# Kernel tuning notes

Measured on AMD Instinct MI355X. Metric: run time of the kernel, lower is better.

The kernel has to match this reference:

```python
import jax, jax.numpy as jnp
import numpy as np

B, S, D = 4, 4096, 512
H = 8
DH = D // H


def setup_inputs() -> dict:
    key = jax.random.key(0)
    k = jax.random.split(key, 5)
    x = jax.random.normal(k[0], (B, S, D), dtype=jnp.float32)
    # in_proj: Linear(D, 3D) with bias; out_proj: Linear(D, D) with bias
    std = 1.0 / np.sqrt(D)
    w_in = jax.random.uniform(k[1], (3 * D, D), minval=-std, maxval=std, dtype=jnp.float32)
    b_in = jax.random.uniform(k[2], (3 * D,), minval=-std, maxval=std, dtype=jnp.float32)
    w_out = jax.random.uniform(k[3], (D, D), minval=-std, maxval=std, dtype=jnp.float32)
    b_out = jax.random.uniform(k[4], (D,), minval=-std, maxval=std, dtype=jnp.float32)
    return {"x": x, "w_in": w_in, "b_in": b_in, "w_out": w_out, "b_out": b_out}


def reference(x, w_in, b_in, w_out, b_out):
    batch, seq_len, d_embed = x.shape
    scale = DH ** 0.5
    qkv = jnp.einsum('bsd,ed->bse', x, w_in) + b_in  # (B, S, 3D)
    q, k, v = jnp.split(qkv, 3, axis=-1)
    # (B, H, S, DH)
    q = q.reshape(batch, seq_len, H, DH).transpose(0, 2, 1, 3)
    k = k.reshape(batch, seq_len, H, DH).transpose(0, 2, 1, 3)
    v = v.reshape(batch, seq_len, H, DH).transpose(0, 2, 1, 3)
    scores = jnp.einsum('bhqd,bhkd->bhqk', q, k) / scale  # full N x N scores
    weights = jax.nn.softmax(scores, axis=-1)
    out = jnp.einsum('bhqk,bhkd->bhqd', weights, v)
    out = out.transpose(0, 2, 1, 3).reshape(batch, seq_len, d_embed)
    out = jnp.einsum('bsd,ed->bse', out, w_out) + b_out
    return out
```

## Files before the change

### kernel.cpp

```cpp
#include <hip/hip_runtime.h>
#include <hip/hip_bf16.h>

typedef short short8 __attribute__((ext_vector_type(8)));
typedef unsigned short ushort8v __attribute__((ext_vector_type(8)));
typedef unsigned short ushort4v __attribute__((ext_vector_type(4)));
typedef float f32x4 __attribute__((ext_vector_type(4)));
typedef unsigned int uint32;

#define USH unsigned short

__device__ __forceinline__ USH f2bf(float f) {
  unsigned int u = __builtin_bit_cast(unsigned int, f);
  u = (u + 0x7FFFu + ((u >> 16) & 1u)) >> 16;
  return (USH)u;
}

__device__ __forceinline__ uint32 pkbf2(float lo, float hi) {
  __hip_bfloat162 h2 = __float22bfloat162_rn(float2{lo, hi});
  uint32 r;
  __builtin_memcpy(&r, &h2, 4);
  return r;
}

__device__ __forceinline__ f32x4 mfma16(short8 a, short8 b, f32x4 c) {
  return __builtin_amdgcn_mfma_f32_16x16x32_bf16(a, b, c, 0, 0, 0);
}

__device__ __forceinline__ void gload16(const USH* g, USH* l) {
  __builtin_amdgcn_global_load_lds(
      (const __attribute__((address_space(1))) unsigned int*)g,
      (__attribute__((address_space(3))) unsigned int*)l, 16, 0, 0);
}

template <int CTRL>
__device__ __forceinline__ float dppmaxstep(float x) {
  int xi = __builtin_bit_cast(int, x);
  int yi = __builtin_amdgcn_update_dpp(xi, xi, CTRL, 0xF, 0xF, true);
  return fmaxf(x, __builtin_bit_cast(float, yi));
}
__device__ __forceinline__ float rowmax16(float x) {
  x = dppmaxstep<0xB1>(x);
  x = dppmaxstep<0x4E>(x);
  x = dppmaxstep<0x141>(x);
  x = dppmaxstep<0x140>(x);
  return x;
}

__device__ __forceinline__ f32x4 vmax4(f32x4 a, f32x4 b) {
  f32x4 r;
  r[0] = fmaxf(a[0], b[0]);
  r[1] = fmaxf(a[1], b[1]);
  r[2] = fmaxf(a[2], b[2]);
  r[3] = fmaxf(a[3], b[3]);
  return r;
}

__global__ __launch_bounds__(256) void cvt_bf16(const float* __restrict__ in,
                                                USH* __restrict__ out, int n4) {
  int i = blockIdx.x * 256 + threadIdx.x;
  if (i >= n4) return;
  f32x4 v = *(const f32x4*)(in + (size_t)i * 4);
  ushort4v o;
#pragma unroll
  for (int k = 0; k < 4; k++) o[k] = f2bf(v[k]);
  *(ushort4v*)(out + (size_t)i * 4) = o;
}

template <bool OUT_F32>
__global__ __launch_bounds__(256) void gemm_bt(const USH* __restrict__ A,
                                               const USH* __restrict__ B,
                                               const float* __restrict__ bias,
                                               void* __restrict__ Cout,
                                               int M, int N, int K) {
  __shared__ __align__(16) USH As[128 * 64];
  __shared__ __align__(16) USH Bs[128 * 64];
  const int tid = threadIdx.x;
  const int row0 = blockIdx.x * 128;
  const int col0 = blockIdx.y * 128;
  const int wid = tid >> 6, lane = tid & 63;
  const int wr = (wid >> 1) * 64, wc = (wid & 1) * 64;
  const int lmod = lane & 15, ldiv = lane >> 4;
  const int asw = lmod & 7;
  const int srow = lane >> 3;
  const int scol = ((lane & 7) ^ srow) * 8;

  f32x4 acc[4][4];
#pragma unroll
  for (int i = 0; i < 4; i++)
#pragma unroll
    for (int j = 0; j < 4; j++) acc[i][j] = (f32x4){0.f, 0.f, 0.f, 0.f};

  const USH* Ab = A + (size_t)row0 * K;
  const USH* Bb = B + (size_t)col0 * K;

  for (int k0 = 0; k0 < K; k0 += 64) {
    __syncthreads();
#pragma unroll
    for (int i = 0; i < 4; i++) {
      int r0 = wid * 32 + i * 8;
      int r = r0 + srow;
      gload16(&Ab[(size_t)r * K + k0 + scol], &As[r0 * 64]);
      gload16(&Bb[(size_t)r * K + k0 + scol], &Bs[r0 * 64]);
    }
    __syncthreads();
#pragma unroll
    for (int kk = 0; kk < 64; kk += 32) {
      short8 a[4], b[4];
#pragma unroll
      for (int i = 0; i < 4; i++)
        a[i] = *(const short8*)&As[(wr + i * 16 + lmod) * 64 +
                                   ((((kk >> 3) + ldiv) ^ asw) << 3)];
#pragma unroll
      for (int i = 0; i < 4; i++)
        b[i] = *(const short8*)&Bs[(wc + i * 16 + lmod) * 64 +
                                   ((((kk >> 3) + ldiv) ^ asw) << 3)];
#pragma unroll
      for (int i = 0; i < 4; i++)
#pragma unroll
        for (int j = 0; j < 4; j++)
          acc[i][j] = mfma16(a[i], b[j], acc[i][j]);
    }
  }

  const int r4 = ldiv * 4;
#pragma unroll
  for (int i = 0; i < 4; i++) {
#pragma unroll
    for (int j = 0; j < 4; j++) {
      int rr = row0 + wr + i * 16 + r4;
      int cc = col0 + wc + j * 16 + lmod;
      float bv = bias[cc];
#pragma unroll
      for (int t = 0; t < 4; t++) {
        float v = acc[i][j][t] + bv;
        if (OUT_F32)
          ((float*)Cout)[(size_t)(rr + t) * N + cc] = v;
        else
          ((USH*)Cout)[(size_t)(rr + t) * N + cc] = f2bf(v);
      }
    }
  }
}

__global__ __launch_bounds__(256) void vtrans(const USH* __restrict__ qkv,
                                              USH* __restrict__ vT) {
  __shared__ __align__(16) USH t[64][72];
  const int bh = blockIdx.y, b = bh >> 3, h = bh & 7;
  const int s0 = blockIdx.x * 64;
  const int tid = threadIdx.x;
  const int r = tid >> 4, c4 = (tid & 15) * 4;
#pragma unroll
  for (int i = 0; i < 4; i++) {
    int row = r + i * 16;
    *(ushort4v*)&t[row][c4] =
        *(const ushort4v*)&qkv[(size_t)(b * 4096 + s0 + row) * 1536 + 1024 + h * 64 + c4];
  }
  __syncthreads();
  const int d = tid >> 2, sb = (tid & 3) * 16;
  size_t ob = (size_t)(bh * 64 + d) * 4096 + s0 + sb;
#pragma unroll
  for (int half = 0; half < 2; half++) {
    ushort8v o;
#pragma unroll
    for (int k = 0; k < 8; k++) o[k] = t[sb + half * 8 + k][d];
    *(ushort8v*)&vT[ob + half * 8] = o;
  }
}

__global__ __launch_bounds__(256, 3) void attn_fwd(const USH* __restrict__ qkv,
                                                   const USH* __restrict__ vT,
                                                   USH* __restrict__ attno) {
  __shared__ __align__(16) USH Ks[2][64 * 64];
  __shared__ __align__(16) USH Vs[2][64 * 64];
  __shared__ __align__(16) USH Ps[4][32 * 64];

  const int fb = blockIdx.x;
  const int b3 = fb & 7;
  const int rest = fb >> 3;
  const int qb = rest & 31;
  const int bh = b3 + 8 * (rest >> 5);
  const int b = bh >> 3, h = bh & 7;

  const int wid = threadIdx.x >> 6, lane = threadIdx.x & 63;
  const int lmod = lane & 15, ldiv = lane >> 4;
  const int ksw = lmod & 7;
  const int qrow0 = qb * 128 + wid * 32;

  short8 qf00, qf01, qf10, qf11;
  {
    const USH* qp = qkv + (size_t)(b * 4096 + qrow0 + lmod) * 1536 + h * 64 + ldiv * 8;
    qf00 = *(const short8*)qp;
    qf01 = *(const short8*)(qp + 32);
    qp += (size_t)16 * 1536;
    qf10 = *(const short8*)qp;
    qf11 = *(const short8*)(qp + 32);
  }

  short8 ones;
#pragma unroll
  for (int i = 0; i < 8; i++) ones[i] = (short)0x3F80;

  f32x4 acc0[4], acc1[4];
#pragma unroll
  for (int n = 0; n < 4; n++) {
    acc0[n] = (f32x4){0.f, 0.f, 0.f, 0.f};
    acc1[n] = (f32x4){0.f, 0.f, 0.f, 0.f};
  }
  f32x4 l0 = (f32x4){0.f, 0.f, 0.f, 0.f}, l1 = l0;
  f32x4 m0 = (f32x4){-1e30f, -1e30f, -1e30f, -1e30f}, m1 = m0;
  f32x4 nmk0 = (f32x4){0.f, 0.f, 0.f, 0.f}, nmk1 = nmk0;
  const f32x4 z4 = (f32x4){0.f, 0.f, 0.f, 0.f};

  const USH* kbase = qkv + (size_t)b * 4096 * 1536 + 512 + h * 64;
  const USH* vbase = vT + (size_t)bh * 64 * 4096;
  const int srow = lane >> 3;
  const int scol = ((lane & 7) ^ srow) * 8;
  const float K2 = 0.18033688011112042f;

  auto stage = [&](int bu, int k0) {
#pragma unroll
    for (int i = 0; i < 2; ++i) {
      int r0 = wid * 16 + i * 8;
      int r = r0 + srow;
      gload16(kbase + (size_t)(k0 + r) * 1536 + scol, &Ks[bu][r0 * 64]);
      gload16(vbase + (size_t)r * 4096 + k0 + scol, &Vs[bu][r0 * 64]);
    }
  };

  stage(0, 0);

  for (int t = 0; t < 64; ++t) {
    const int cur = t & 1;
    __syncthreads();
    if (t < 63) stage(cur ^ 1, (t + 1) * 64);

    const USH* Kc = &Ks[cur][0];
    const USH* Vc = &Vs[cur][0];
    USH* Pw = &Ps[wid][0];

    f32x4 s0[4], s1[4];
#pragma unroll
    for (int n = 0; n < 4; n++) {
      const USH* kr = Kc + (n * 16 + lmod) * 64;
      short8 kf0 = *(const short8*)(kr + ((ldiv ^ ksw) << 3));
      short8 kf1 = *(const short8*)(kr + (((4 + ldiv) ^ ksw) << 3));
      s0[n] = mfma16(qf00, kf0, z4);
      s0[n] = mfma16(qf01, kf1, s0[n]);
      s1[n] = mfma16(qf10, kf0, z4);
      s1[n] = mfma16(qf11, kf1, s1[n]);
    }

    f32x4 pm0 = vmax4(vmax4(s0[0], s0[1]), vmax4(s0[2], s0[3]));
    f32x4 pm1 = vmax4(vmax4(s1[0], s1[1]), vmax4(s1[2], s1[3]));
    bool ok = true;
#pragma unroll
    for (int j = 0; j < 4; j++)
      ok = ok && (pm0[j] <= m0[j] + 64.f) && (pm1[j] <= m1[j] + 64.f);
    if (!__all(ok)) {
      f32x4 al0, al1;
#pragma unroll
      for (int j = 0; j < 4; j++) {
        float v = rowmax16(pm0[j]);
        float mn = fmaxf(m0[j], v);
        al0[j] = __builtin_amdgcn_exp2f((m0[j] - mn) * K2);
        m0[j] = mn;
        nmk0[j] = -mn * K2;
      }
#pragma unroll
      for (int j = 0; j < 4; j++) {
        float v = rowmax16(pm1[j]);
        float mn = fmaxf(m1[j], v);
        al1[j] = __builtin_amdgcn_exp2f((m1[j] - mn) * K2);
        m1[j] = mn;
        nmk1[j] = -mn * K2;
      }
#pragma unroll
      for (int n = 0; n < 4; n++) {
        acc0[n] *= al0;
        acc1[n] *= al1;
      }
      l0 *= al0;
      l1 *= al1;
    }

#pragma unroll
    for (int n = 0; n < 4; n++) {
      const int col = n * 16 + lmod;
#pragma unroll
      for (int jp = 0; jp < 2; jp++) {
        const int r = ldiv * 4 + jp * 2;
        {
          float e0 = __builtin_amdgcn_exp2f(fmaf(s0[n][jp * 2], K2, nmk0[jp * 2]));
          float e1 = __builtin_amdgcn_exp2f(fmaf(s0[n][jp * 2 + 1], K2, nmk0[jp * 2 + 1]));
          uint32 pr = pkbf2(e0, e1);
          Pw[(r * 64 + col) ^ ((r & 7) << 3)] = (USH)pr;
          Pw[((r + 1) * 64 + col) ^ (((r + 1) & 7) << 3)] = (USH)(pr >> 16);
        }
        {
          float e0 = __builtin_amdgcn_exp2f(fmaf(s1[n][jp * 2], K2, nmk1[jp * 2]));
          float e1 = __builtin_amdgcn_exp2f(fmaf(s1[n][jp * 2 + 1], K2, nmk1[jp * 2 + 1]));
          uint32 pr = pkbf2(e0, e1);
          Pw[((16 + r) * 64 + col) ^ ((r & 7) << 3)] = (USH)pr;
          Pw[((17 + r) * 64 + col) ^ (((r + 1) & 7) << 3)] = (USH)(pr >> 16);
        }
      }
    }

#pragma unroll
    for (int kc = 0; kc < 2; kc++) {
      const int off = kc * 32 + ldiv * 8;
      short8 pf0 = *(const short8*)&Pw[(lmod * 64 + off) ^ (ksw << 3)];
      short8 pf1 = *(const short8*)&Pw[((16 + lmod) * 64 + off) ^ (ksw << 3)];
      l0 = mfma16(pf0, ones, l0);
      l1 = mfma16(pf1, ones, l1);
#pragma unroll
      for (int n = 0; n < 4; n++) {
        const USH* vr = Vc + (n * 16 + lmod) * 64;
        short8 vf = *(const short8*)(vr + (((kc * 4 + ldiv) ^ ksw) << 3));
        acc0[n] = mfma16(pf0, vf, acc0[n]);
        acc1[n] = mfma16(pf1, vf, acc1[n]);
      }
    }
  }

  float iv0[4], iv1[4];
#pragma unroll
  for (int j = 0; j < 4; j++) {
    iv0[j] = 1.0f / l0[j];
    iv1[j] = 1.0f / l1[j];
  }
  USH* ob = attno + (size_t)(b * 4096 + qrow0) * 512 + h * 64;
#pragma unroll
  for (int n = 0; n < 4; n++) {
#pragma unroll
    for (int j = 0; j < 4; j++) {
      ob[(size_t)(ldiv * 4 + j) * 512 + n * 16 + lmod] = f2bf(acc0[n][j] * iv0[j]);
      ob[(size_t)(16 + ldiv * 4 + j) * 512 + n * 16 + lmod] = f2bf(acc1[n][j] * iv1[j]);
    }
  }
}

extern "C" void kernel_launch(void* const* d_in, const int* in_sizes, int n_in,
                              void* d_out, int out_size, void* d_ws, size_t ws_size,
                              hipStream_t stream) {
  const float* x = (const float*)d_in[0];
  const float* w_in = (const float*)d_in[1];
  const float* b_in = (const float*)d_in[2];
  const float* w_out = (const float*)d_in[3];
  const float* b_out = (const float*)d_in[4];
  float* out = (float*)d_out;

  char* ws = (char*)d_ws;
  USH* xb = (USH*)(ws);
  USH* winb = (USH*)(ws + 16777216);
  USH* woutb = (USH*)(ws + 18350080);
  USH* qkv = (USH*)(ws + 18874368);
  USH* vT = (USH*)(ws + 69206016);
  USH* attno = xb;

  cvt_bf16<<<8192, 256, 0, stream>>>(x, xb, 2097152);
  cvt_bf16<<<768, 256, 0, stream>>>(w_in, winb, 196608);
  cvt_bf16<<<256, 256, 0, stream>>>(w_out, woutb, 65536);

  gemm_bt<false><<<dim3(128, 12), 256, 0, stream>>>(xb, winb, b_in, qkv, 16384, 1536, 512);
  vtrans<<<dim3(64, 32), 256, 0, stream>>>(qkv, vT);
  attn_fwd<<<1024, 256, 0, stream>>>(qkv, vT, attno);
  gemm_bt<true><<<dim3(128, 4), 256, 0, stream>>>(attno, woutb, b_out, out, 16384, 512, 512);
}
```

Measured before the change: 287.8 us.

## Halve attention query tile per wave to raise occupancy

Each wave now processes 16 query rows instead of 32, so each block covers 64 queries and the grid doubles. Launch bounds are raised to allow four blocks per CU and the P staging buffer shrinks accordingly. This is meant to cut register pressure and improve occupancy and wave balance. In exchange, each staged K/V tile is reused by half as many queries, which doubles K/V global and LDS traffic per unit of work.

```diff
diff --git a/kernel.cpp b/kernel.cpp
--- a/kernel.cpp
+++ b/kernel.cpp
@@ -167,48 +167,41 @@
   }
 }
 
-__global__ __launch_bounds__(256, 3) void attn_fwd(const USH* __restrict__ qkv,
+__global__ __launch_bounds__(256, 4) void attn_fwd(const USH* __restrict__ qkv,
                                                    const USH* __restrict__ vT,
                                                    USH* __restrict__ attno) {
   __shared__ __align__(16) USH Ks[2][64 * 64];
   __shared__ __align__(16) USH Vs[2][64 * 64];
-  __shared__ __align__(16) USH Ps[4][32 * 64];
+  __shared__ __align__(16) USH Ps[4][16 * 64];
 
   const int fb = blockIdx.x;
   const int b3 = fb & 7;
   const int rest = fb >> 3;
-  const int qb = rest & 31;
-  const int bh = b3 + 8 * (rest >> 5);
+  const int qb = rest & 63;
+  const int bh = b3 + 8 * (rest >> 6);
   const int b = bh >> 3, h = bh & 7;
 
   const int wid = threadIdx.x >> 6, lane = threadIdx.x & 63;
   const int lmod = lane & 15, ldiv = lane >> 4;
   const int ksw = lmod & 7;
-  const int qrow0 = qb * 128 + wid * 32;
-
-  short8 qf00, qf01, qf10, qf11;
+  const int qrow0 = qb * 64 + wid * 16;
+
+  short8 qf0, qf1;
   {
     const USH* qp = qkv + (size_t)(b * 4096 + qrow0 + lmod) * 1536 + h * 64 + ldiv * 8;
-    qf00 = *(const short8*)qp;
-    qf01 = *(const short8*)(qp + 32);
-    qp += (size_t)16 * 1536;
-    qf10 = *(const short8*)qp;
-    qf11 = *(const short8*)(qp + 32);
+    qf0 = *(const short8*)qp;
+    qf1 = *(const short8*)(qp + 32);
   }
 
   short8 ones;
 #pragma unroll
   for (int i = 0; i < 8; i++) ones[i] = (short)0x3F80;
 
-  f32x4 acc0[4], acc1[4];
-#pragma unroll
-  for (int n = 0; n < 4; n++) {
-    acc0[n] = (f32x4){0.f, 0.f, 0.f, 0.f};
-    acc1[n] = (f32x4){0.f, 0.f, 0.f, 0.f};
-  }
-  f32x4 l0 = (f32x4){0.f, 0.f, 0.f, 0.f}, l1 = l0;
-  f32x4 m0 = (f32x4){-1e30f, -1e30f, -1e30f, -1e30f}, m1 = m0;
-  f32x4 nmk0 = (f32x4){0.f, 0.f, 0.f, 0.f}, nmk1 = nmk0;
+  f32x4 acc[4];
+#pragma unroll
+  for (int n = 0; n < 4; n++) acc[n] = (f32x4){0.f, 0.f, 0.f, 0.f};
+  f32x4 l = (f32x4){0.f, 0.f, 0.f, 0.f};
+  f32x4 m = (f32x4){-1e30f, -1e30f, -1e30f, -1e30f};
   const f32x4 z4 = (f32x4){0.f, 0.f, 0.f, 0.f};
 
   const USH* kbase = qkv + (size_t)b * 4096 * 1536 + 512 + h * 64;
@@ -238,50 +231,36 @@
     const USH* Vc = &Vs[cur][0];
     USH* Pw = &Ps[wid][0];
 
-    f32x4 s0[4], s1[4];
+    f32x4 s[4];
 #pragma unroll
     for (int n = 0; n < 4; n++) {
       const USH* kr = Kc + (n * 16 + lmod) * 64;
       short8 kf0 = *(const short8*)(kr + ((ldiv ^ ksw) << 3));
       short8 kf1 = *(const short8*)(kr + (((4 + ldiv) ^ ksw) << 3));
-      s0[n] = mfma16(qf00, kf0, z4);
-      s0[n] = mfma16(qf01, kf1, s0[n]);
-      s1[n] = mfma16(qf10, kf0, z4);
-      s1[n] = mfma16(qf11, kf1, s1[n]);
-    }
-
-    f32x4 pm0 = vmax4(vmax4(s0[0], s0[1]), vmax4(s0[2], s0[3]));
-    f32x4 pm1 = vmax4(vmax4(s1[0], s1[1]), vmax4(s1[2], s1[3]));
+      s[n] = mfma16(qf0, kf0, z4);
+      s[n] = mfma16(qf1, kf1, s[n]);
+    }
+
+    f32x4 pm = vmax4(vmax4(s[0], s[1]), vmax4(s[2], s[3]));
     bool ok = true;
 #pragma unroll
-    for (int j = 0; j < 4; j++)
-      ok = ok && (pm0[j] <= m0[j] + 64.f) && (pm1[j] <= m1[j] + 64.f);
+    for (int j = 0; j < 4; j++) ok = ok && (pm[j] <= m[j] + 64.f);
     if (!__all(ok)) {
-      f32x4 al0, al1;
+      f32x4 al;
 #pragma unroll
       for (int j = 0; j < 4; j++) {
-        float v = rowmax16(pm0[j]);
-        float mn = fmaxf(m0[j], v);
-        al0[j] = __builtin_amdgcn_exp2f((m0[j] - mn) * K2);
-        m0[j] = mn;
-        nmk0[j] = -mn * K2;
+        float v = rowmax16(pm[j]);
+        float mn = fmaxf(m[j], v);
+        al[j] = __builtin_amdgcn_exp2f((m[j] - mn) * K2);
+        m[j] = mn;
       }
 #pragma unroll
-      for (int j = 0; j < 4; j++) {
-        float v = rowmax16(pm1[j]);
-        float mn = fmaxf(m1[j], v);
-        al1[j] = __builtin_amdgcn_exp2f((m1[j] - mn) * K2);
-        m1[j] = mn;
-        nmk1[j] = -mn * K2;
-      }
-#pragma unroll
-      for (int n = 0; n < 4; n++) {
-        acc0[n] *= al0;
-        acc1[n] *= al1;
-      }
-      l0 *= al0;
-      l1 *= al1;
-    }
+      for (int n = 0; n < 4; n++) acc[n] *= al;
+      l *= al;
+    }
+    f32x4 nmk;
+#pragma unroll
+    for (int j = 0; j < 4; j++) nmk[j] = -m[j] * K2;
 
 #pragma unroll
     for (int n = 0; n < 4; n++) {
@@ -289,53 +268,37 @@
 #pragma unroll
       for (int jp = 0; jp < 2; jp++) {
         const int r = ldiv * 4 + jp * 2;
-        {
-          float e0 = __builtin_amdgcn_exp2f(fmaf(s0[n][jp * 2], K2, nmk0[jp * 2]));
-          float e1 = __builtin_amdgcn_exp2f(fmaf(s0[n][jp * 2 + 1], K2, nmk0[jp * 2 + 1]));
-          uint32 pr = pkbf2(e0, e1);
-          Pw[(r * 64 + col) ^ ((r & 7) << 3)] = (USH)pr;
-          Pw[((r + 1) * 64 + col) ^ (((r + 1) & 7) << 3)] = (USH)(pr >> 16);
-        }
-        {
-          float e0 = __builtin_amdgcn_exp2f(fmaf(s1[n][jp * 2], K2, nmk1[jp * 2]));
-          float e1 = __builtin_amdgcn_exp2f(fmaf(s1[n][jp * 2 + 1], K2, nmk1[jp * 2 + 1]));
-          uint32 pr = pkbf2(e0, e1);
-          Pw[((16 + r) * 64 + col) ^ ((r & 7) << 3)] = (USH)pr;
-          Pw[((17 + r) * 64 + col) ^ (((r + 1) & 7) << 3)] = (USH)(pr >> 16);
-        }
+        float e0 = __builtin_amdgcn_exp2f(fmaf(s[n][jp * 2], K2, nmk[jp * 2]));
+        float e1 = __builtin_amdgcn_exp2f(fmaf(s[n][jp * 2 + 1], K2, nmk[jp * 2 + 1]));
+        uint32 pr = pkbf2(e0, e1);
+        Pw[(r * 64 + col) ^ ((r & 7) << 3)] = (USH)pr;
+        Pw[((r + 1) * 64 + col) ^ (((r + 1) & 7) << 3)] = (USH)(pr >> 16);
       }
     }
 
 #pragma unroll
     for (int kc = 0; kc < 2; kc++) {
       const int off = kc * 32 + ldiv * 8;
-      short8 pf0 = *(const short8*)&Pw[(lmod * 64 + off) ^ (ksw << 3)];
-      short8 pf1 = *(const short8*)&Pw[((16 + lmod) * 64 + off) ^ (ksw << 3)];
-      l0 = mfma16(pf0, ones, l0);
-      l1 = mfma16(pf1, ones, l1);
+      short8 pf = *(const short8*)&Pw[(lmod * 64 + off) ^ (ksw << 3)];
+      l = mfma16(pf, ones, l);
 #pragma unroll
       for (int n = 0; n < 4; n++) {
         const USH* vr = Vc + (n * 16 + lmod) * 64;
         short8 vf = *(const short8*)(vr + (((kc * 4 + ldiv) ^ ksw) << 3));
-        acc0[n] = mfma16(pf0, vf, acc0[n]);
-        acc1[n] = mfma16(pf1, vf, acc1[n]);
+        acc[n] = mfma16(pf, vf, acc[n]);
       }
     }
   }
 
-  float iv0[4], iv1[4];
-#pragma unroll
-  for (int j = 0; j < 4; j++) {
-    iv0[j] = 1.0f / l0[j];
-    iv1[j] = 1.0f / l1[j];
-  }
+  float iv[4];
+#pragma unroll
+  for (int j = 0; j < 4; j++) iv[j] = 1.0f / l[j];
   USH* ob = attno + (size_t)(b * 4096 + qrow0) * 512 + h * 64;
 #pragma unroll
   for (int n = 0; n < 4; n++) {
 #pragma unroll
     for (int j = 0; j < 4; j++) {
-      ob[(size_t)(ldiv * 4 + j) * 512 + n * 16 + lmod] = f2bf(acc0[n][j] * iv0[j]);
-      ob[(size_t)(16 + ldiv * 4 + j) * 512 + n * 16 + lmod] = f2bf(acc1[n][j] * iv1[j]);
+      ob[(size_t)(ldiv * 4 + j) * 512 + n * 16 + lmod] = f2bf(acc[n][j] * iv[j]);
     }
   }
 }
@@ -364,6 +327,6 @@
 
   gemm_bt<false><<<dim3(128, 12), 256, 0, stream>>>(xb, winb, b_in, qkv, 16384, 1536, 512);
   vtrans<<<dim3(64, 32), 256, 0, stream>>>(qkv, vT);
-  attn_fwd<<<1024, 256, 0, stream>>>(qkv, vT, attno);
+  attn_fwd<<<2048, 256, 0, stream>>>(qkv, vT, attno);
   gemm_bt<true><<<dim3(128, 4), 256, 0, stream>>>(attno, woutb, b_out, out, 16384, 512, 512);
 }
```

New measurement: 311.6 us. +8.3%, slower.
